# Kernel optimization log

Hardware: AMD Instinct MI355X
Metric: run time of the kernel (lower is better)

## Reference

```python
import jax, jax.numpy as jnp
import numpy as np

D = 512
B = 8
S1 = 2048
S2 = 2048


def _rope_cos_sin(seq_len, dim, dtype=jnp.float32):
    half = dim // 2
    inv_freq = 1.0 / (10000.0 ** (jnp.arange(half, dtype=jnp.float32) / half))
    t = jnp.arange(seq_len, dtype=jnp.float32)
    freqs = jnp.outer(t, inv_freq)                      # [S, D/2]
    emb = jnp.concatenate([freqs, freqs], axis=-1)      # [S, D]
    return jnp.cos(emb).astype(dtype), jnp.sin(emb).astype(dtype)


def _rotate_half(x):
    half = x.shape[-1] // 2
    return jnp.concatenate([-x[..., half:], x[..., :half]], axis=-1)


def _apply_rope(x, cos, sin):
    # x: [B, S, D]; cos/sin: [S, D]
    return x * cos[None, :, :] + _rotate_half(x) * sin[None, :, :]


def setup_inputs() -> dict:
    key = jax.random.key(0)
    ks = jax.random.split(key, 12)
    s = 1.0 / np.sqrt(D)
    return {
        "h1": jax.random.normal(ks[0], (B, S1, D), dtype=jnp.float32),
        "h2": jax.random.normal(ks[1], (B, S2, D), dtype=jnp.float32),
        "Wq": jax.random.normal(ks[2], (D, D), dtype=jnp.float32) * s,
        "bq": jnp.zeros((D,), dtype=jnp.float32),
        "Wk": jax.random.normal(ks[3], (D, D), dtype=jnp.float32) * s,
        "bk": jnp.zeros((D,), dtype=jnp.float32),
        "Wv": jax.random.normal(ks[4], (D, D), dtype=jnp.float32) * s,
        "bv": jnp.zeros((D,), dtype=jnp.float32),
        "Wo": jax.random.normal(ks[5], (D, D), dtype=jnp.float32) * s,
        "bo": jnp.zeros((D,), dtype=jnp.float32),
    }


def reference(h1, h2, Wq, bq, Wk, bk, Wv, bv, Wo, bo):
    d = h1.shape[-1]
    # Linear projections (torch Linear: x @ W.T + b)
    q = jnp.einsum("bsd,ed->bse", h1, Wq) + bq
    k = jnp.einsum("bsd,ed->bse", h2, Wk) + bk
    v = jnp.einsum("bsd,ed->bse", h2, Wv) + bv
    # RoPE on full hidden dim (single head)
    cos_q, sin_q = _rope_cos_sin(q.shape[1], d)
    cos_k, sin_k = _rope_cos_sin(k.shape[1], d)
    q = _apply_rope(q, cos_q, sin_q)
    k = _apply_rope(k, cos_k, sin_k)
    # scaled dot-product attention with full score matrix (faithful to source)
    energy = jnp.einsum("bqd,bkd->bqk", q, k) / jnp.sqrt(jnp.float32(d))
    attn = jax.nn.softmax(energy, axis=-1)
    out = jnp.einsum("bqk,bkd->bqd", attn, v)
    return jnp.einsum("bsd,ed->bse", out, Wo) + bo
```

## Files before the change

### kernel.cpp

```cpp
#include <hip/hip_runtime.h>
#include <stdint.h>

#define SCALE_E 0.044194173824159216f
#define LOG2_10000 13.287712379549449f
#define MCONST 8.0f

typedef __bf16 bf16x8 __attribute__((ext_vector_type(8)));
typedef float  f32x4  __attribute__((ext_vector_type(4)));

#define MFMA16(a, b, c) __builtin_amdgcn_mfma_f32_16x16x32_bf16((a), (b), (c), 0, 0, 0)

__device__ __forceinline__ void gload_lds16(const void* gp, void* lp) {
  __builtin_amdgcn_global_load_lds(
      reinterpret_cast<const uint32_t __attribute__((address_space(1)))*>(
          reinterpret_cast<uintptr_t>(gp)),
      reinterpret_cast<uint32_t __attribute__((address_space(3)))*>(
          reinterpret_cast<uintptr_t>(lp)),
      16, 0, 0);
}

__global__ __launch_bounds__(256) void gemm_split(
    const float* __restrict__ A, const float* __restrict__ W,
    const float* __restrict__ bias, float* __restrict__ C, int M)
{
  __shared__ __align__(16) __bf16 Als[2 * 512 * 8];
  __shared__ __align__(16) __bf16 Wls[2 * 512 * 8];

  const int t    = threadIdx.x;
  const int lane = t & 63;
  const int w    = t >> 6;
  const int m    = lane & 15;
  const int quad = lane >> 4;
  const int mw   = w & 1;
  const int nw   = w >> 1;
  const int m0   = blockIdx.y * 128;
  const int n0   = blockIdx.x * 128;

  const float* Ap0 = A + (size_t)(m0 + w * 16 + m) * 512 + quad * 8;
  const float* Ap1 = A + (size_t)(m0 + (w + 4) * 16 + m) * 512 + quad * 8;
  const float* Wp0 = W + (size_t)(n0 + w * 16 + m) * 512 + quad * 8;
  const float* Wp1 = W + (size_t)(n0 + (w + 4) * 16 + m) * 512 + quad * 8;

  f32x4 acc[4][4] = {};

  float4 ra[4], rw_[4];
  ra[0] = *(const float4*)(Ap0);     ra[1] = *(const float4*)(Ap0 + 4);
  ra[2] = *(const float4*)(Ap1);     ra[3] = *(const float4*)(Ap1 + 4);
  rw_[0] = *(const float4*)(Wp0);    rw_[1] = *(const float4*)(Wp0 + 4);
  rw_[2] = *(const float4*)(Wp1);    rw_[3] = *(const float4*)(Wp1 + 4);

  for (int kt = 0; kt < 512; kt += 32) {
    __syncthreads();
    #pragma unroll
    for (int h = 0; h < 2; ++h) {
      int slot = t + 256 * h;
      float v[8] = {ra[2*h].x, ra[2*h].y, ra[2*h].z, ra[2*h].w,
                    ra[2*h+1].x, ra[2*h+1].y, ra[2*h+1].z, ra[2*h+1].w};
      float u[8] = {rw_[2*h].x, rw_[2*h].y, rw_[2*h].z, rw_[2*h].w,
                    rw_[2*h+1].x, rw_[2*h+1].y, rw_[2*h+1].z, rw_[2*h+1].w};
      bf16x8 ah, al, bh, bl;
      #pragma unroll
      for (int j = 0; j < 8; ++j) {
        __bf16 hv = (__bf16)v[j];
        ah[j] = hv; al[j] = (__bf16)(v[j] - (float)hv);
        __bf16 hu = (__bf16)u[j];
        bh[j] = hu; bl[j] = (__bf16)(u[j] - (float)hu);
      }
      *(bf16x8*)&Als[(size_t)slot * 8]         = ah;
      *(bf16x8*)&Als[(size_t)(512 + slot) * 8] = al;
      *(bf16x8*)&Wls[(size_t)slot * 8]         = bh;
      *(bf16x8*)&Wls[(size_t)(512 + slot) * 8] = bl;
    }
    __syncthreads();

    if (kt + 32 < 512) {
      ra[0] = *(const float4*)(Ap0 + kt + 32);  ra[1] = *(const float4*)(Ap0 + kt + 36);
      ra[2] = *(const float4*)(Ap1 + kt + 32);  ra[3] = *(const float4*)(Ap1 + kt + 36);
      rw_[0] = *(const float4*)(Wp0 + kt + 32); rw_[1] = *(const float4*)(Wp0 + kt + 36);
      rw_[2] = *(const float4*)(Wp1 + kt + 32); rw_[3] = *(const float4*)(Wp1 + kt + 36);
    }

    bf16x8 ah[4], al[4], bh[4], bl[4];
    #pragma unroll
    for (int mt = 0; mt < 4; ++mt) {
      ah[mt] = *(const bf16x8*)&Als[(size_t)((mw * 4 + mt) * 64 + lane) * 8];
      al[mt] = *(const bf16x8*)&Als[(size_t)(512 + (mw * 4 + mt) * 64 + lane) * 8];
    }
    #pragma unroll
    for (int nt = 0; nt < 4; ++nt) {
      bh[nt] = *(const bf16x8*)&Wls[(size_t)((nw * 4 + nt) * 64 + lane) * 8];
      bl[nt] = *(const bf16x8*)&Wls[(size_t)(512 + (nw * 4 + nt) * 64 + lane) * 8];
    }
    #pragma unroll
    for (int mt = 0; mt < 4; ++mt)
      #pragma unroll
      for (int nt = 0; nt < 4; ++nt) {
        acc[mt][nt] = MFMA16(al[mt], bh[nt], acc[mt][nt]);
        acc[mt][nt] = MFMA16(ah[mt], bl[nt], acc[mt][nt]);
        acc[mt][nt] = MFMA16(ah[mt], bh[nt], acc[mt][nt]);
      }
  }

  float bv[4];
  #pragma unroll
  for (int nt = 0; nt < 4; ++nt) bv[nt] = bias[n0 + (nw * 4 + nt) * 16 + m];

  #pragma unroll
  for (int mt = 0; mt < 4; ++mt)
    #pragma unroll
    for (int r = 0; r < 4; ++r) {
      size_t row = m0 + (mw * 4 + mt) * 16 + quad * 4 + r;
      float* cp = C + row * 512 + n0;
      #pragma unroll
      for (int nt = 0; nt < 4; ++nt)
        cp[(nw * 4 + nt) * 16 + m] = acc[mt][nt][r] + bv[nt];
    }
}

__global__ __launch_bounds__(256) void rope_cast(
    const float* __restrict__ X, __bf16* __restrict__ Y, float scale)
{
  const int row = blockIdx.x;
  const int s = row & 2047;
  const int j = threadIdx.x;
  const float* p = X + (size_t)row * 512;
  __bf16* q = Y + (size_t)row * 512;
  float invf = exp2f((float)j * (-LOG2_10000 / 256.0f));
  float ang = (float)s * invf;
  float c = cosf(ang), sn = sinf(ang);
  float x1 = p[j], x2 = p[j + 256];
  q[j]       = (__bf16)((x1 * c - x2 * sn) * scale);
  q[j + 256] = (__bf16)((x2 * c + x1 * sn) * scale);
}

__global__ __launch_bounds__(256) void cast_transpose_v(
    const float* __restrict__ V, __bf16* __restrict__ Vt)
{
  __shared__ float tile[32][33];
  const int b  = blockIdx.z;
  const int s0 = blockIdx.x * 32;
  const int d0 = blockIdx.y * 32;
  const float* Vb = V + (size_t)b * 2048 * 512;
  __bf16* Vtb = Vt + (size_t)b * 512 * 2048;

  #pragma unroll
  for (int r = 0; r < 4; ++r) {
    int s = s0 + threadIdx.y + 8 * r;
    tile[threadIdx.y + 8 * r][threadIdx.x] = Vb[(size_t)s * 512 + d0 + threadIdx.x];
  }
  __syncthreads();
  #pragma unroll
  for (int r = 0; r < 4; ++r) {
    int d = d0 + threadIdx.y + 8 * r;
    Vtb[(size_t)d * 2048 + s0 + threadIdx.x] = (__bf16)tile[threadIdx.x][threadIdx.y + 8 * r];
  }
}

__global__ __launch_bounds__(512, 2) void attn_mfma(
    const __bf16* __restrict__ Qb, const __bf16* __restrict__ Kb,
    const __bf16* __restrict__ Vt, float* __restrict__ O)
{
  __shared__ __align__(16) __bf16 Kbuf[4096 * 8];
  __shared__ __align__(16) __bf16 Ps[4096];
  __shared__ float l_sh[128];

  const int t    = threadIdx.x;
  const int b    = blockIdx.x & 7;
  const int q0   = (blockIdx.x >> 3) * 64;
  const int w    = t >> 6;
  const int lane = t & 63;
  const int m    = lane & 15;
  const int quad = lane >> 4;
  const int rw   = w >> 1;
  const int kp   = w & 1;

  const __bf16* Kbase = Kb + (size_t)b * 2048 * 512;
  const __bf16* Vbase = Vt + (size_t)b * 512 * 2048;

  const __bf16* qrow = Qb + ((size_t)b * 2048 + q0 + rw * 16 + m) * 512 + quad * 8;
  bf16x8 qf[16];
  #pragma unroll
  for (int kb = 0; kb < 16; ++kb) qf[kb] = *(const bf16x8*)(qrow + kb * 32);

  bf16x8 onesf;
  #pragma unroll
  for (int j = 0; j < 8; ++j) onesf[j] = (__bf16)1.0f;

  f32x4 o_acc[4][4] = {};
  f32x4 l_tile = {0.f, 0.f, 0.f, 0.f};

  const __bf16* vrow = Vbase + (size_t)(w * 64 + m) * 2048;

  const __bf16* lsrc = &Ps[(size_t)((rw * 2 + kp) * 64 + lane) * 8];

  #pragma unroll
  for (int i = 0; i < 8; ++i) {
    const int j = w * 8 + i;
    gload_lds16(Kbase + (size_t)((j & 3) * 16 + m) * 512 + (j >> 2) * 32 + quad * 8,
                &Kbuf[(size_t)(j * 64 + lane) * 8]);
  }

  for (int kt = 0; kt < 2048; kt += 64) {
    __syncthreads();

    bf16x8 vf[8];
    #pragma unroll
    for (int dt = 0; dt < 4; ++dt)
      #pragma unroll
      for (int kh = 0; kh < 2; ++kh)
        vf[dt * 2 + kh] =
            *(const bf16x8*)(vrow + (size_t)dt * 16 * 2048 + kt + kh * 32 + quad * 8);

    f32x4 sc0 = {0.f, 0.f, 0.f, 0.f}, sc1 = {0.f, 0.f, 0.f, 0.f};
    __builtin_amdgcn_s_setprio(1);
    #pragma unroll
    for (int kb = 0; kb < 16; ++kb) {
      bf16x8 k0 = *(const bf16x8*)&Kbuf[(size_t)((kb * 4 + kp * 2 + 0) * 64 + lane) * 8];
      bf16x8 k1 = *(const bf16x8*)&Kbuf[(size_t)((kb * 4 + kp * 2 + 1) * 64 + lane) * 8];
      sc0 = MFMA16(qf[kb], k0, sc0);
      sc1 = MFMA16(qf[kb], k1, sc1);
    }
    __builtin_amdgcn_s_setprio(0);

    #pragma unroll
    for (int g = 0; g < 2; ++g) {
      const int kg = kp * 2 + g;
      f32x4 sc = g ? sc1 : sc0;
      float p0 = __expf(sc[0] - MCONST);
      float p1 = __expf(sc[1] - MCONST);
      float p2 = __expf(sc[2] - MCONST);
      float p3 = __expf(sc[3] - MCONST);
      __bf16* pw = &Ps[(size_t)(((rw * 2 + (kg >> 1)) * 4 + ((kg & 1) * 2 + (m >> 3))) * 16
                                + quad * 4) * 8 + (m & 7)];
      pw[0]  = (__bf16)p0;
      pw[8]  = (__bf16)p1;
      pw[16] = (__bf16)p2;
      pw[24] = (__bf16)p3;
    }

    __syncthreads();

    if (kt + 64 < 2048) {
      #pragma unroll
      for (int i = 0; i < 8; ++i) {
        const int j = w * 8 + i;
        gload_lds16(Kbase + (size_t)(kt + 64 + (j & 3) * 16 + m) * 512 + (j >> 2) * 32 + quad * 8,
                    &Kbuf[(size_t)(j * 64 + lane) * 8]);
      }
    }

    __builtin_amdgcn_s_setprio(1);

    {
      bf16x8 lf = *(const bf16x8*)lsrc;
      l_tile = MFMA16(lf, onesf, l_tile);
    }

    #pragma unroll
    for (int kh = 0; kh < 2; ++kh) {
      bf16x8 pf0 = *(const bf16x8*)&Ps[(size_t)((0 * 2 + kh) * 64 + lane) * 8];
      bf16x8 pf1 = *(const bf16x8*)&Ps[(size_t)((1 * 2 + kh) * 64 + lane) * 8];
      bf16x8 pf2 = *(const bf16x8*)&Ps[(size_t)((2 * 2 + kh) * 64 + lane) * 8];
      bf16x8 pf3 = *(const bf16x8*)&Ps[(size_t)((3 * 2 + kh) * 64 + lane) * 8];
      #pragma unroll
      for (int dt = 0; dt < 4; ++dt) {
        bf16x8 vv = vf[dt * 2 + kh];
        o_acc[0][dt] = MFMA16(pf0, vv, o_acc[0][dt]);
        o_acc[1][dt] = MFMA16(pf1, vv, o_acc[1][dt]);
        o_acc[2][dt] = MFMA16(pf2, vv, o_acc[2][dt]);
        o_acc[3][dt] = MFMA16(pf3, vv, o_acc[3][dt]);
      }
    }
    __builtin_amdgcn_s_setprio(0);
  }

  if (m == 0) {
    #pragma unroll
    for (int r = 0; r < 4; ++r)
      l_sh[kp * 64 + rw * 16 + quad * 4 + r] = l_tile[r];
  }
  __syncthreads();
  #pragma unroll
  for (int rt = 0; rt < 4; ++rt) {
    float invl[4];
    #pragma unroll
    for (int r = 0; r < 4; ++r)
      invl[r] = 1.0f / (l_sh[rt * 16 + quad * 4 + r] + l_sh[64 + rt * 16 + quad * 4 + r]);
    #pragma unroll
    for (int dt = 0; dt < 4; ++dt)
      #pragma unroll
      for (int r = 0; r < 4; ++r) {
        size_t row = (size_t)b * 2048 + q0 + rt * 16 + quad * 4 + r;
        O[row * 512 + w * 64 + dt * 16 + m] = o_acc[rt][dt][r] * invl[r];
      }
  }
}

extern "C" void kernel_launch(void* const* d_in, const int* in_sizes, int n_in,
                              void* d_out, int out_size, void* d_ws, size_t ws_size,
                              hipStream_t stream)
{
  const float* h1 = (const float*)d_in[0];
  const float* h2 = (const float*)d_in[1];
  const float* Wq = (const float*)d_in[2];
  const float* bq = (const float*)d_in[3];
  const float* Wk = (const float*)d_in[4];
  const float* bk = (const float*)d_in[5];
  const float* Wv = (const float*)d_in[6];
  const float* bv = (const float*)d_in[7];
  const float* Wo = (const float*)d_in[8];
  const float* bo = (const float*)d_in[9];
  float* out = (float*)d_out;

  const size_t MB = 1024 * 1024;

  float*  Qf  = (float*)d_ws;
  float*  Kf  = (float*)((char*)d_ws + 32 * MB);
  float*  O2  = (float*)((char*)d_ws + 16 * MB);
  __bf16* Vtb = (__bf16*)d_ws;
  __bf16* Qbb = (__bf16*)((char*)d_ws + 64 * MB);
  __bf16* Kbb = (__bf16*)((char*)d_ws + 80 * MB);
  float*  Vf  = out;

  const int M = 8 * 2048;
  dim3 gG(4, M / 128);

  gemm_split<<<gG, 256, 0, stream>>>(h1, Wq, bq, Qf, M);
  gemm_split<<<gG, 256, 0, stream>>>(h2, Wk, bk, Kf, M);
  gemm_split<<<gG, 256, 0, stream>>>(h2, Wv, bv, Vf, M);
  rope_cast<<<M, 256, 0, stream>>>(Qf, Qbb, SCALE_E);
  rope_cast<<<M, 256, 0, stream>>>(Kf, Kbb, 1.0f);
  cast_transpose_v<<<dim3(64, 16, 8), dim3(32, 8), 0, stream>>>(Vf, Vtb);
  attn_mfma<<<256, 512, 0, stream>>>(Qbb, Kbb, Vtb, O2);
  gemm_split<<<gG, 256, 0, stream>>>(O2, Wo, bo, out, M);
}
```

Baseline: 418.1 us.

## Double attention key tile to 128 and split V loads across the softmax barrier

Each iteration of the attention loop now processes 128 keys instead of 64, so the number of block barriers and loop iterations is halved. Each wave computes four score tiles per step, and the K and P shared-memory buffers double in size. Half of the V fragments are now loaded after the softmax barrier to spread register pressure and hide latency. The larger LDS footprint (about 144 KB) and the extra registers may reduce occupancy below the two blocks per CU requested.

```diff
diff --git a/kernel.cpp b/kernel.cpp
--- a/kernel.cpp
+++ b/kernel.cpp
@@ -160,9 +160,9 @@
     const __bf16* __restrict__ Qb, const __bf16* __restrict__ Kb,
     const __bf16* __restrict__ Vt, float* __restrict__ O)
 {
-  __shared__ __align__(16) __bf16 Kbuf[4096 * 8];
-  __shared__ __align__(16) __bf16 Ps[4096];
-  __shared__ float l_sh[128];
+  __shared__ __align__(16) __bf16 Kbuf[8192 * 8];
+  __shared__ __align__(16) __bf16 Ps[8192];
+  __shared__ float l_sh[256];
 
   const int t    = threadIdx.x;
   const int b    = blockIdx.x & 7;
@@ -187,64 +187,81 @@
   for (int j = 0; j < 8; ++j) onesf[j] = (__bf16)1.0f;
 
   f32x4 o_acc[4][4] = {};
-  f32x4 l_tile = {0.f, 0.f, 0.f, 0.f};
+  f32x4 l_t0 = {0.f, 0.f, 0.f, 0.f};
+  f32x4 l_t1 = {0.f, 0.f, 0.f, 0.f};
 
   const __bf16* vrow = Vbase + (size_t)(w * 64 + m) * 2048;
 
-  const __bf16* lsrc = &Ps[(size_t)((rw * 2 + kp) * 64 + lane) * 8];
-
-  #pragma unroll
-  for (int i = 0; i < 8; ++i) {
-    const int j = w * 8 + i;
-    gload_lds16(Kbase + (size_t)((j & 3) * 16 + m) * 512 + (j >> 2) * 32 + quad * 8,
+  const __bf16* lsrc0 = &Ps[(size_t)((rw * 4 + kp * 2 + 0) * 64 + lane) * 8];
+  const __bf16* lsrc1 = &Ps[(size_t)((rw * 4 + kp * 2 + 1) * 64 + lane) * 8];
+
+  #define SM_STORE(scv, kg_) {                                                  \
+    float p0 = __expf((scv)[0] - MCONST);                                       \
+    float p1 = __expf((scv)[1] - MCONST);                                       \
+    float p2 = __expf((scv)[2] - MCONST);                                       \
+    float p3 = __expf((scv)[3] - MCONST);                                       \
+    __bf16* pw = &Ps[(size_t)(((rw * 4 + ((kg_) >> 1)) * 4 +                    \
+                               (((kg_) & 1) * 2 + (m >> 3))) * 16 + quad * 4)   \
+                     * 8 + (m & 7)];                                            \
+    pw[0]  = (__bf16)p0;                                                        \
+    pw[8]  = (__bf16)p1;                                                        \
+    pw[16] = (__bf16)p2;                                                        \
+    pw[24] = (__bf16)p3;                                                        \
+  }
+
+  #pragma unroll
+  for (int i = 0; i < 16; ++i) {
+    const int j = w * 16 + i;
+    gload_lds16(Kbase + (size_t)((j & 7) * 16 + m) * 512 + (j >> 3) * 32 + quad * 8,
                 &Kbuf[(size_t)(j * 64 + lane) * 8]);
   }
 
-  for (int kt = 0; kt < 2048; kt += 64) {
+  for (int kt = 0; kt < 2048; kt += 128) {
     __syncthreads();
 
-    bf16x8 vf[8];
+    bf16x8 vf[16];
     #pragma unroll
     for (int dt = 0; dt < 4; ++dt)
       #pragma unroll
       for (int kh = 0; kh < 2; ++kh)
-        vf[dt * 2 + kh] =
+        vf[dt * 4 + kh] =
             *(const bf16x8*)(vrow + (size_t)dt * 16 * 2048 + kt + kh * 32 + quad * 8);
 
     f32x4 sc0 = {0.f, 0.f, 0.f, 0.f}, sc1 = {0.f, 0.f, 0.f, 0.f};
+    f32x4 sc2 = {0.f, 0.f, 0.f, 0.f}, sc3 = {0.f, 0.f, 0.f, 0.f};
     __builtin_amdgcn_s_setprio(1);
     #pragma unroll
     for (int kb = 0; kb < 16; ++kb) {
-      bf16x8 k0 = *(const bf16x8*)&Kbuf[(size_t)((kb * 4 + kp * 2 + 0) * 64 + lane) * 8];
-      bf16x8 k1 = *(const bf16x8*)&Kbuf[(size_t)((kb * 4 + kp * 2 + 1) * 64 + lane) * 8];
+      bf16x8 k0 = *(const bf16x8*)&Kbuf[(size_t)((kb * 8 + kp * 4 + 0) * 64 + lane) * 8];
+      bf16x8 k1 = *(const bf16x8*)&Kbuf[(size_t)((kb * 8 + kp * 4 + 1) * 64 + lane) * 8];
+      bf16x8 k2 = *(const bf16x8*)&Kbuf[(size_t)((kb * 8 + kp * 4 + 2) * 64 + lane) * 8];
+      bf16x8 k3 = *(const bf16x8*)&Kbuf[(size_t)((kb * 8 + kp * 4 + 3) * 64 + lane) * 8];
       sc0 = MFMA16(qf[kb], k0, sc0);
       sc1 = MFMA16(qf[kb], k1, sc1);
+      sc2 = MFMA16(qf[kb], k2, sc2);
+      sc3 = MFMA16(qf[kb], k3, sc3);
     }
     __builtin_amdgcn_s_setprio(0);
 
-    #pragma unroll
-    for (int g = 0; g < 2; ++g) {
-      const int kg = kp * 2 + g;
-      f32x4 sc = g ? sc1 : sc0;
-      float p0 = __expf(sc[0] - MCONST);
-      float p1 = __expf(sc[1] - MCONST);
-      float p2 = __expf(sc[2] - MCONST);
-      float p3 = __expf(sc[3] - MCONST);
-      __bf16* pw = &Ps[(size_t)(((rw * 2 + (kg >> 1)) * 4 + ((kg & 1) * 2 + (m >> 3))) * 16
-                                + quad * 4) * 8 + (m & 7)];
-      pw[0]  = (__bf16)p0;
-      pw[8]  = (__bf16)p1;
-      pw[16] = (__bf16)p2;
-      pw[24] = (__bf16)p3;
-    }
+    SM_STORE(sc0, kp * 4 + 0);
+    SM_STORE(sc1, kp * 4 + 1);
+    SM_STORE(sc2, kp * 4 + 2);
+    SM_STORE(sc3, kp * 4 + 3);
 
     __syncthreads();
 
-    if (kt + 64 < 2048) {
-      #pragma unroll
-      for (int i = 0; i < 8; ++i) {
-        const int j = w * 8 + i;
-        gload_lds16(Kbase + (size_t)(kt + 64 + (j & 3) * 16 + m) * 512 + (j >> 2) * 32 + quad * 8,
+    #pragma unroll
+    for (int dt = 0; dt < 4; ++dt)
+      #pragma unroll
+      for (int kh = 2; kh < 4; ++kh)
+        vf[dt * 4 + kh] =
+            *(const bf16x8*)(vrow + (size_t)dt * 16 * 2048 + kt + kh * 32 + quad * 8);
+
+    if (kt + 128 < 2048) {
+      #pragma unroll
+      for (int i = 0; i < 16; ++i) {
+        const int j = w * 16 + i;
+        gload_lds16(Kbase + (size_t)(kt + 128 + (j & 7) * 16 + m) * 512 + (j >> 3) * 32 + quad * 8,
                     &Kbuf[(size_t)(j * 64 + lane) * 8]);
       }
     }
@@ -252,19 +269,21 @@
     __builtin_amdgcn_s_setprio(1);
 
     {
-      bf16x8 lf = *(const bf16x8*)lsrc;
-      l_tile = MFMA16(lf, onesf, l_tile);
-    }
-
-    #pragma unroll
-    for (int kh = 0; kh < 2; ++kh) {
-      bf16x8 pf0 = *(const bf16x8*)&Ps[(size_t)((0 * 2 + kh) * 64 + lane) * 8];
-      bf16x8 pf1 = *(const bf16x8*)&Ps[(size_t)((1 * 2 + kh) * 64 + lane) * 8];
-      bf16x8 pf2 = *(const bf16x8*)&Ps[(size_t)((2 * 2 + kh) * 64 + lane) * 8];
-      bf16x8 pf3 = *(const bf16x8*)&Ps[(size_t)((3 * 2 + kh) * 64 + lane) * 8];
+      bf16x8 lf0 = *(const bf16x8*)lsrc0;
+      bf16x8 lf1 = *(const bf16x8*)lsrc1;
+      l_t0 = MFMA16(lf0, onesf, l_t0);
+      l_t1 = MFMA16(lf1, onesf, l_t1);
+    }
+
+    #pragma unroll
+    for (int kh = 0; kh < 4; ++kh) {
+      bf16x8 pf0 = *(const bf16x8*)&Ps[(size_t)((0 * 4 + kh) * 64 + lane) * 8];
+      bf16x8 pf1 = *(const bf16x8*)&Ps[(size_t)((1 * 4 + kh) * 64 + lane) * 8];
+      bf16x8 pf2 = *(const bf16x8*)&Ps[(size_t)((2 * 4 + kh) * 64 + lane) * 8];
+      bf16x8 pf3 = *(const bf16x8*)&Ps[(size_t)((3 * 4 + kh) * 64 + lane) * 8];
       #pragma unroll
       for (int dt = 0; dt < 4; ++dt) {
-        bf16x8 vv = vf[dt * 2 + kh];
+        bf16x8 vv = vf[dt * 4 + kh];
         o_acc[0][dt] = MFMA16(pf0, vv, o_acc[0][dt]);
         o_acc[1][dt] = MFMA16(pf1, vv, o_acc[1][dt]);
         o_acc[2][dt] = MFMA16(pf2, vv, o_acc[2][dt]);
@@ -276,8 +295,10 @@
 
   if (m == 0) {
     #pragma unroll
-    for (int r = 0; r < 4; ++r)
-      l_sh[kp * 64 + rw * 16 + quad * 4 + r] = l_tile[r];
+    for (int r = 0; r < 4; ++r) {
+      l_sh[(kp * 2 + 0) * 64 + rw * 16 + quad * 4 + r] = l_t0[r];
+      l_sh[(kp * 2 + 1) * 64 + rw * 16 + quad * 4 + r] = l_t1[r];
+    }
   }
   __syncthreads();
   #pragma unroll
@@ -285,7 +306,10 @@
     float invl[4];
     #pragma unroll
     for (int r = 0; r < 4; ++r)
-      invl[r] = 1.0f / (l_sh[rt * 16 + quad * 4 + r] + l_sh[64 + rt * 16 + quad * 4 + r]);
+      invl[r] = 1.0f / (l_sh[0 * 64 + rt * 16 + quad * 4 + r]
+                      + l_sh[1 * 64 + rt * 16 + quad * 4 + r]
+                      + l_sh[2 * 64 + rt * 16 + quad * 4 + r]
+                      + l_sh[3 * 64 + rt * 16 + quad * 4 + r]);
     #pragma unroll
     for (int dt = 0; dt < 4; ++dt)
       #pragma unroll
```

Result: no change. 421.4 us (+0.8%).

## Halve attention query tile to 32 rows with 4-wave blocks, doubling grid size

Applied to the files above, without the earlier changes.

The attention kernel now processes 32 query rows per block with 256 threads (4 waves) instead of 64 rows with 512 threads, launching 512 blocks instead of 256. Each wave covers 128 output columns rather than 64, and V fragment loads are split into two halves, the second issued after the barrier to spread register pressure and overlap with the K prefetch. More blocks should fill the GPU's compute units better. The cost is that K tiles are reloaded twice as often per query row, raising K traffic per query, and each wave holds more accumulators.

```diff
diff --git a/kernel.cpp b/kernel.cpp
--- a/kernel.cpp
+++ b/kernel.cpp
@@ -156,17 +156,17 @@
   }
 }
 
-__global__ __launch_bounds__(512, 2) void attn_mfma(
+__global__ __launch_bounds__(256, 2) void attn_mfma(
     const __bf16* __restrict__ Qb, const __bf16* __restrict__ Kb,
     const __bf16* __restrict__ Vt, float* __restrict__ O)
 {
   __shared__ __align__(16) __bf16 Kbuf[4096 * 8];
-  __shared__ __align__(16) __bf16 Ps[4096];
-  __shared__ float l_sh[128];
+  __shared__ __align__(16) __bf16 Ps[2048];
+  __shared__ float l_sh[64];
 
   const int t    = threadIdx.x;
   const int b    = blockIdx.x & 7;
-  const int q0   = (blockIdx.x >> 3) * 64;
+  const int q0   = (blockIdx.x >> 3) * 32;
   const int w    = t >> 6;
   const int lane = t & 63;
   const int m    = lane & 15;
@@ -186,16 +186,30 @@
   #pragma unroll
   for (int j = 0; j < 8; ++j) onesf[j] = (__bf16)1.0f;
 
-  f32x4 o_acc[4][4] = {};
+  f32x4 o_acc[2][8] = {};
   f32x4 l_tile = {0.f, 0.f, 0.f, 0.f};
 
-  const __bf16* vrow = Vbase + (size_t)(w * 64 + m) * 2048;
-
-  const __bf16* lsrc = &Ps[(size_t)((rw * 2 + kp) * 64 + lane) * 8];
-
-  #pragma unroll
-  for (int i = 0; i < 8; ++i) {
-    const int j = w * 8 + i;
+  const __bf16* vrow = Vbase + (size_t)(w * 128 + m) * 2048;
+
+  const __bf16* lsrc = &Ps[(size_t)(w * 64 + lane) * 8];
+
+  #define SM_STORE(scv, kg_) {                                                  \
+    float p0 = __expf((scv)[0] - MCONST);                                       \
+    float p1 = __expf((scv)[1] - MCONST);                                       \
+    float p2 = __expf((scv)[2] - MCONST);                                       \
+    float p3 = __expf((scv)[3] - MCONST);                                       \
+    __bf16* pw = &Ps[(size_t)(((rw * 2 + ((kg_) >> 1)) * 4 +                    \
+                               (((kg_) & 1) * 2 + (m >> 3))) * 16 + quad * 4)   \
+                     * 8 + (m & 7)];                                            \
+    pw[0]  = (__bf16)p0;                                                        \
+    pw[8]  = (__bf16)p1;                                                        \
+    pw[16] = (__bf16)p2;                                                        \
+    pw[24] = (__bf16)p3;                                                        \
+  }
+
+  #pragma unroll
+  for (int i = 0; i < 16; ++i) {
+    const int j = w * 16 + i;
     gload_lds16(Kbase + (size_t)((j & 3) * 16 + m) * 512 + (j >> 2) * 32 + quad * 8,
                 &Kbuf[(size_t)(j * 64 + lane) * 8]);
   }
@@ -203,13 +217,10 @@
   for (int kt = 0; kt < 2048; kt += 64) {
     __syncthreads();
 
-    bf16x8 vf[8];
-    #pragma unroll
-    for (int dt = 0; dt < 4; ++dt)
-      #pragma unroll
-      for (int kh = 0; kh < 2; ++kh)
-        vf[dt * 2 + kh] =
-            *(const bf16x8*)(vrow + (size_t)dt * 16 * 2048 + kt + kh * 32 + quad * 8);
+    bf16x8 vf0[8];
+    #pragma unroll
+    for (int dt = 0; dt < 8; ++dt)
+      vf0[dt] = *(const bf16x8*)(vrow + (size_t)dt * 16 * 2048 + kt + quad * 8);
 
     f32x4 sc0 = {0.f, 0.f, 0.f, 0.f}, sc1 = {0.f, 0.f, 0.f, 0.f};
     __builtin_amdgcn_s_setprio(1);
@@ -222,28 +233,20 @@
     }
     __builtin_amdgcn_s_setprio(0);
 
-    #pragma unroll
-    for (int g = 0; g < 2; ++g) {
-      const int kg = kp * 2 + g;
-      f32x4 sc = g ? sc1 : sc0;
-      float p0 = __expf(sc[0] - MCONST);
-      float p1 = __expf(sc[1] - MCONST);
-      float p2 = __expf(sc[2] - MCONST);
-      float p3 = __expf(sc[3] - MCONST);
-      __bf16* pw = &Ps[(size_t)(((rw * 2 + (kg >> 1)) * 4 + ((kg & 1) * 2 + (m >> 3))) * 16
-                                + quad * 4) * 8 + (m & 7)];
-      pw[0]  = (__bf16)p0;
-      pw[8]  = (__bf16)p1;
-      pw[16] = (__bf16)p2;
-      pw[24] = (__bf16)p3;
-    }
+    SM_STORE(sc0, kp * 2 + 0);
+    SM_STORE(sc1, kp * 2 + 1);
 
     __syncthreads();
 
+    bf16x8 vf1[8];
+    #pragma unroll
+    for (int dt = 0; dt < 8; ++dt)
+      vf1[dt] = *(const bf16x8*)(vrow + (size_t)dt * 16 * 2048 + kt + 32 + quad * 8);
+
     if (kt + 64 < 2048) {
       #pragma unroll
-      for (int i = 0; i < 8; ++i) {
-        const int j = w * 8 + i;
+      for (int i = 0; i < 16; ++i) {
+        const int j = w * 16 + i;
         gload_lds16(Kbase + (size_t)(kt + 64 + (j & 3) * 16 + m) * 512 + (j >> 2) * 32 + quad * 8,
                     &Kbuf[(size_t)(j * 64 + lane) * 8]);
       }
@@ -256,19 +259,22 @@
       l_tile = MFMA16(lf, onesf, l_tile);
     }
 
-    #pragma unroll
-    for (int kh = 0; kh < 2; ++kh) {
-      bf16x8 pf0 = *(const bf16x8*)&Ps[(size_t)((0 * 2 + kh) * 64 + lane) * 8];
-      bf16x8 pf1 = *(const bf16x8*)&Ps[(size_t)((1 * 2 + kh) * 64 + lane) * 8];
-      bf16x8 pf2 = *(const bf16x8*)&Ps[(size_t)((2 * 2 + kh) * 64 + lane) * 8];
-      bf16x8 pf3 = *(const bf16x8*)&Ps[(size_t)((3 * 2 + kh) * 64 + lane) * 8];
-      #pragma unroll
-      for (int dt = 0; dt < 4; ++dt) {
-        bf16x8 vv = vf[dt * 2 + kh];
-        o_acc[0][dt] = MFMA16(pf0, vv, o_acc[0][dt]);
-        o_acc[1][dt] = MFMA16(pf1, vv, o_acc[1][dt]);
-        o_acc[2][dt] = MFMA16(pf2, vv, o_acc[2][dt]);
-        o_acc[3][dt] = MFMA16(pf3, vv, o_acc[3][dt]);
+    {
+      bf16x8 pf0 = *(const bf16x8*)&Ps[(size_t)((0 * 2 + 0) * 64 + lane) * 8];
+      bf16x8 pf1 = *(const bf16x8*)&Ps[(size_t)((1 * 2 + 0) * 64 + lane) * 8];
+      #pragma unroll
+      for (int dt = 0; dt < 8; ++dt) {
+        o_acc[0][dt] = MFMA16(pf0, vf0[dt], o_acc[0][dt]);
+        o_acc[1][dt] = MFMA16(pf1, vf0[dt], o_acc[1][dt]);
+      }
+    }
+    {
+      bf16x8 pf0 = *(const bf16x8*)&Ps[(size_t)((0 * 2 + 1) * 64 + lane) * 8];
+      bf16x8 pf1 = *(const bf16x8*)&Ps[(size_t)((1 * 2 + 1) * 64 + lane) * 8];
+      #pragma unroll
+      for (int dt = 0; dt < 8; ++dt) {
+        o_acc[0][dt] = MFMA16(pf0, vf1[dt], o_acc[0][dt]);
+        o_acc[1][dt] = MFMA16(pf1, vf1[dt], o_acc[1][dt]);
       }
     }
     __builtin_amdgcn_s_setprio(0);
@@ -277,21 +283,21 @@
   if (m == 0) {
     #pragma unroll
     for (int r = 0; r < 4; ++r)
-      l_sh[kp * 64 + rw * 16 + quad * 4 + r] = l_tile[r];
+      l_sh[(w & 1) * 32 + (w >> 1) * 16 + quad * 4 + r] = l_tile[r];
   }
   __syncthreads();
   #pragma unroll
-  for (int rt = 0; rt < 4; ++rt) {
+  for (int rt = 0; rt < 2; ++rt) {
     float invl[4];
     #pragma unroll
     for (int r = 0; r < 4; ++r)
-      invl[r] = 1.0f / (l_sh[rt * 16 + quad * 4 + r] + l_sh[64 + rt * 16 + quad * 4 + r]);
-    #pragma unroll
-    for (int dt = 0; dt < 4; ++dt)
+      invl[r] = 1.0f / (l_sh[rt * 16 + quad * 4 + r] + l_sh[32 + rt * 16 + quad * 4 + r]);
+    #pragma unroll
+    for (int dt = 0; dt < 8; ++dt)
       #pragma unroll
       for (int r = 0; r < 4; ++r) {
         size_t row = (size_t)b * 2048 + q0 + rt * 16 + quad * 4 + r;
-        O[row * 512 + w * 64 + dt * 16 + m] = o_acc[rt][dt][r] * invl[r];
+        O[row * 512 + w * 128 + dt * 16 + m] = o_acc[rt][dt][r] * invl[r];
       }
   }
 }
@@ -331,6 +337,6 @@
   rope_cast<<<M, 256, 0, stream>>>(Qf, Qbb, SCALE_E);
   rope_cast<<<M, 256, 0, stream>>>(Kf, Kbb, 1.0f);
   cast_transpose_v<<<dim3(64, 16, 8), dim3(32, 8), 0, stream>>>(Vf, Vtb);
-  attn_mfma<<<256, 512, 0, stream>>>(Qbb, Kbb, Vtb, O2);
+  attn_mfma<<<512, 256, 0, stream>>>(Qbb, Kbb, Vtb, O2);
   gemm_split<<<gG, 256, 0, stream>>>(O2, Wo, bo, out, M);
 }
```

Result: slower. 524.3 us (+25.4%).

## Fuse RoPE into Q/K projection GEMM epilogue via interleaved weight rows

Applied to the files above, without the earlier changes.

Adds a prep kernel that permutes the Wq/Wk rows (and biases) so that each rotated pair (i, i+256) lands in adjacent output columns, and precomputes a cos/sin table. The Q/K GEMMs then apply RoPE in the epilogue using a lane shuffle and write bf16 directly. This removes the fp32 Q/K round trips through global memory and the two separate rope_cast launches. Q and K now come out in a permuted feature order, which is consistent for Q·K but adds an extra prep launch and table lookups in the epilogue.

```diff
diff --git a/kernel.cpp b/kernel.cpp
--- a/kernel.cpp
+++ b/kernel.cpp
@@ -17,6 +17,34 @@
       reinterpret_cast<uint32_t __attribute__((address_space(3)))*>(
           reinterpret_cast<uintptr_t>(lp)),
       16, 0, 0);
+}
+
+__global__ __launch_bounds__(256) void rope_prep(
+    const float* __restrict__ Wq, const float* __restrict__ bq,
+    const float* __restrict__ Wk, const float* __restrict__ bk,
+    float* __restrict__ Wqp, float* __restrict__ bqp,
+    float* __restrict__ Wkp, float* __restrict__ bkp,
+    float2* __restrict__ tab)
+{
+  const int bid = blockIdx.x, t = threadIdx.x;
+  if (bid < 1024) {
+    const float* W  = (bid < 512) ? Wq  : Wk;
+    const float* bb = (bid < 512) ? bq  : bk;
+    float* Wp       = (bid < 512) ? Wqp : Wkp;
+    float* bp       = (bid < 512) ? bqp : bkp;
+    const int e    = bid & 511;
+    const int orig = (e >> 1) + (e & 1) * 256;
+    const float2* s = (const float2*)(W + (size_t)orig * 512);
+    float2* d       = (float2*)(Wp + (size_t)e * 512);
+    d[t] = s[t];
+    if (t == 0) bp[e] = bb[orig];
+  } else {
+    const int s = bid - 1024;
+    const int i = t;
+    float invf = exp2f((float)i * (-LOG2_10000 / 256.0f));
+    float ang  = (float)s * invf;
+    tab[(size_t)s * 256 + i] = make_float2(cosf(ang), sinf(ang));
+  }
 }
 
 __global__ __launch_bounds__(256) void gemm_split(
@@ -117,20 +145,117 @@
     }
 }
 
-__global__ __launch_bounds__(256) void rope_cast(
-    const float* __restrict__ X, __bf16* __restrict__ Y, float scale)
-{
-  const int row = blockIdx.x;
-  const int s = row & 2047;
-  const int j = threadIdx.x;
-  const float* p = X + (size_t)row * 512;
-  __bf16* q = Y + (size_t)row * 512;
-  float invf = exp2f((float)j * (-LOG2_10000 / 256.0f));
-  float ang = (float)s * invf;
-  float c = cosf(ang), sn = sinf(ang);
-  float x1 = p[j], x2 = p[j + 256];
-  q[j]       = (__bf16)((x1 * c - x2 * sn) * scale);
-  q[j + 256] = (__bf16)((x2 * c + x1 * sn) * scale);
+__global__ __launch_bounds__(256) void gemm_rope(
+    const float* __restrict__ A, const float* __restrict__ W,
+    const float* __restrict__ bias, __bf16* __restrict__ Y,
+    const float2* __restrict__ tab, float scale, int M)
+{
+  __shared__ __align__(16) __bf16 Als[2 * 512 * 8];
+  __shared__ __align__(16) __bf16 Wls[2 * 512 * 8];
+
+  const int t    = threadIdx.x;
+  const int lane = t & 63;
+  const int w    = t >> 6;
+  const int m    = lane & 15;
+  const int quad = lane >> 4;
+  const int mw   = w & 1;
+  const int nw   = w >> 1;
+  const int m0   = blockIdx.y * 128;
+  const int n0   = blockIdx.x * 128;
+
+  const float* Ap0 = A + (size_t)(m0 + w * 16 + m) * 512 + quad * 8;
+  const float* Ap1 = A + (size_t)(m0 + (w + 4) * 16 + m) * 512 + quad * 8;
+  const float* Wp0 = W + (size_t)(n0 + w * 16 + m) * 512 + quad * 8;
+  const float* Wp1 = W + (size_t)(n0 + (w + 4) * 16 + m) * 512 + quad * 8;
+
+  f32x4 acc[4][4] = {};
+
+  float4 ra[4], rw_[4];
+  ra[0] = *(const float4*)(Ap0);     ra[1] = *(const float4*)(Ap0 + 4);
+  ra[2] = *(const float4*)(Ap1);     ra[3] = *(const float4*)(Ap1 + 4);
+  rw_[0] = *(const float4*)(Wp0);    rw_[1] = *(const float4*)(Wp0 + 4);
+  rw_[2] = *(const float4*)(Wp1);    rw_[3] = *(const float4*)(Wp1 + 4);
+
+  for (int kt = 0; kt < 512; kt += 32) {
+    __syncthreads();
+    #pragma unroll
+    for (int h = 0; h < 2; ++h) {
+      int slot = t + 256 * h;
+      float v[8] = {ra[2*h].x, ra[2*h].y, ra[2*h].z, ra[2*h].w,
+                    ra[2*h+1].x, ra[2*h+1].y, ra[2*h+1].z, ra[2*h+1].w};
+      float u[8] = {rw_[2*h].x, rw_[2*h].y, rw_[2*h].z, rw_[2*h].w,
+                    rw_[2*h+1].x, rw_[2*h+1].y, rw_[2*h+1].z, rw_[2*h+1].w};
+      bf16x8 ah, al, bh, bl;
+      #pragma unroll
+      for (int j = 0; j < 8; ++j) {
+        __bf16 hv = (__bf16)v[j];
+        ah[j] = hv; al[j] = (__bf16)(v[j] - (float)hv);
+        __bf16 hu = (__bf16)u[j];
+        bh[j] = hu; bl[j] = (__bf16)(u[j] - (float)hu);
+      }
+      *(bf16x8*)&Als[(size_t)slot * 8]         = ah;
+      *(bf16x8*)&Als[(size_t)(512 + slot) * 8] = al;
+      *(bf16x8*)&Wls[(size_t)slot * 8]         = bh;
+      *(bf16x8*)&Wls[(size_t)(512 + slot) * 8] = bl;
+    }
+    __syncthreads();
+
+    if (kt + 32 < 512) {
+      ra[0] = *(const float4*)(Ap0 + kt + 32);  ra[1] = *(const float4*)(Ap0 + kt + 36);
+      ra[2] = *(const float4*)(Ap1 + kt + 32);  ra[3] = *(const float4*)(Ap1 + kt + 36);
+      rw_[0] = *(const float4*)(Wp0 + kt + 32); rw_[1] = *(const float4*)(Wp0 + kt + 36);
+      rw_[2] = *(const float4*)(Wp1 + kt + 32); rw_[3] = *(const float4*)(Wp1 + kt + 36);
+    }
+
+    bf16x8 ah[4], al[4], bh[4], bl[4];
+    #pragma unroll
+    for (int mt = 0; mt < 4; ++mt) {
+      ah[mt] = *(const bf16x8*)&Als[(size_t)((mw * 4 + mt) * 64 + lane) * 8];
+      al[mt] = *(const bf16x8*)&Als[(size_t)(512 + (mw * 4 + mt) * 64 + lane) * 8];
+    }
+    #pragma unroll
+    for (int nt = 0; nt < 4; ++nt) {
+      bh[nt] = *(const bf16x8*)&Wls[(size_t)((nw * 4 + nt) * 64 + lane) * 8];
+      bl[nt] = *(const bf16x8*)&Wls[(size_t)(512 + (nw * 4 + nt) * 64 + lane) * 8];
+    }
+    #pragma unroll
+    for (int mt = 0; mt < 4; ++mt)
+      #pragma unroll
+      for (int nt = 0; nt < 4; ++nt) {
+        acc[mt][nt] = MFMA16(al[mt], bh[nt], acc[mt][nt]);
+        acc[mt][nt] = MFMA16(ah[mt], bl[nt], acc[mt][nt]);
+        acc[mt][nt] = MFMA16(ah[mt], bh[nt], acc[mt][nt]);
+      }
+  }
+
+  float bv[4];
+  int   ip[4];
+  #pragma unroll
+  for (int nt = 0; nt < 4; ++nt) {
+    int col = n0 + (nw * 4 + nt) * 16 + m;
+    bv[nt] = bias[col];
+    ip[nt] = col >> 1;
+  }
+  const int half = m & 1;
+
+  #pragma unroll
+  for (int mt = 0; mt < 4; ++mt)
+    #pragma unroll
+    for (int r = 0; r < 4; ++r) {
+      int row  = m0 + (mw * 4 + mt) * 16 + quad * 4 + r;
+      int srow = row & 2047;
+      const float2* trow = tab + ((size_t)srow << 8);
+      __bf16* yp = Y + (size_t)row * 512 + n0;
+      #pragma unroll
+      for (int nt = 0; nt < 4; ++nt) {
+        float v  = acc[mt][nt][r] + bv[nt];
+        float px = __shfl_xor(v, 1);
+        float2 cs = trow[ip[nt]];
+        float out = half ? (v * cs.x + px * cs.y)
+                         : (v * cs.x - px * cs.y);
+        yp[(nw * 4 + nt) * 16 + m] = (__bf16)(out * scale);
+      }
+    }
 }
 
 __global__ __launch_bounds__(256) void cast_transpose_v(
@@ -314,10 +439,13 @@
 
   const size_t MB = 1024 * 1024;
 
-  float*  Qf  = (float*)d_ws;
-  float*  Kf  = (float*)((char*)d_ws + 32 * MB);
+  __bf16* Vtb = (__bf16*)d_ws;
   float*  O2  = (float*)((char*)d_ws + 16 * MB);
-  __bf16* Vtb = (__bf16*)d_ws;
+  float*  Wqp = (float*)((char*)d_ws + 48 * MB);
+  float*  Wkp = (float*)((char*)d_ws + 49 * MB);
+  float*  bqp = (float*)((char*)d_ws + 50 * MB);
+  float*  bkp = (float*)((char*)d_ws + 50 * MB + 4096);
+  float2* tab = (float2*)((char*)d_ws + 52 * MB);
   __bf16* Qbb = (__bf16*)((char*)d_ws + 64 * MB);
   __bf16* Kbb = (__bf16*)((char*)d_ws + 80 * MB);
   float*  Vf  = out;
@@ -325,11 +453,10 @@
   const int M = 8 * 2048;
   dim3 gG(4, M / 128);
 
-  gemm_split<<<gG, 256, 0, stream>>>(h1, Wq, bq, Qf, M);
-  gemm_split<<<gG, 256, 0, stream>>>(h2, Wk, bk, Kf, M);
+  rope_prep<<<3072, 256, 0, stream>>>(Wq, bq, Wk, bk, Wqp, bqp, Wkp, bkp, tab);
+  gemm_rope<<<gG, 256, 0, stream>>>(h1, Wqp, bqp, Qbb, tab, SCALE_E, M);
+  gemm_rope<<<gG, 256, 0, stream>>>(h2, Wkp, bkp, Kbb, tab, 1.0f, M);
   gemm_split<<<gG, 256, 0, stream>>>(h2, Wv, bv, Vf, M);
-  rope_cast<<<M, 256, 0, stream>>>(Qf, Qbb, SCALE_E);
-  rope_cast<<<M, 256, 0, stream>>>(Kf, Kbb, 1.0f);
   cast_transpose_v<<<dim3(64, 16, 8), dim3(32, 8), 0, stream>>>(Vf, Vtb);
   attn_mfma<<<256, 512, 0, stream>>>(Qbb, Kbb, Vtb, O2);
   gemm_split<<<gG, 256, 0, stream>>>(O2, Wo, bo, out, M);
```

Result: faster. 405.5 us (-3.0%).
